# Optimization experiments

Hardware: AMD Instinct MI355X
Metric: run time of the kernel (lower is better)

Reference implementation:

```python
import jax, jax.numpy as jnp
import numpy as np

B, S, H, NH = 2, 2048, 1024, 16
HD = H // NH  # 64
SCALE = HD ** -0.5


def setup_inputs() -> dict:
    key = jax.random.key(0)
    k1, k2, k3 = jax.random.split(key, 3)
    x = jax.random.normal(k1, (B, S, H), dtype=jnp.float32)
    w_qkv = jax.random.normal(k2, (H, 3 * H), dtype=jnp.float32) * (H ** -0.5)
    b_qkv = jnp.zeros((3 * H,), dtype=jnp.float32)
    w_out = jax.random.normal(k3, (H, H), dtype=jnp.float32) * (H ** -0.5)
    b_out = jnp.zeros((H,), dtype=jnp.float32)
    return {"x": x, "w_qkv": w_qkv, "b_qkv": b_qkv, "w_out": w_out, "b_out": b_out}


def reference(x, w_qkv, b_qkv, w_out, b_out):
    # qkv projection: [B,S,3H] -> split -> [B,NH,S,HD] each
    qkv = x @ w_qkv + b_qkv
    q, k, v = jnp.split(qkv, 3, axis=-1)
    def heads(t):
        return t.reshape(B, S, NH, HD).transpose(0, 2, 1, 3)  # [B,NH,S,HD]
    q, k, v = heads(q), heads(k), heads(v)
    # full (non-causal) softmax attention; chunking in the original is
    # math-equivalent since each query row attends over all keys
    scores = jnp.einsum('bhqd,bhkd->bhqk', q, k) * SCALE
    attn = jax.nn.softmax(scores, axis=-1)
    out = jnp.einsum('bhqk,bhkd->bhqd', attn, v)  # [B,NH,S,HD]
    out = out.transpose(0, 2, 1, 3).reshape(B, S, H)
    # to_out linear (Dropout is identity in eval mode)
    return out @ w_out + b_out
```

## Files before the change

kernel.cpp:

```cpp
#include <hip/hip_runtime.h>
#include <cstdint>

using u16 = unsigned short;
typedef __bf16 bf16x8 __attribute__((ext_vector_type(8)));
typedef __bf16 bf16x4 __attribute__((ext_vector_type(4)));
typedef float f32x4 __attribute__((ext_vector_type(4)));

#define MFMA16(a, b, c) __builtin_amdgcn_mfma_f32_16x16x32_bf16((a), (b), (c), 0, 0, 0)

__device__ __forceinline__ u16 f2bf(float f) {
  union { float f; uint32_t u; } c; c.f = f;
  uint32_t u = c.u;
  u += 0x7fffu + ((u >> 16) & 1u);
  return (u16)(u >> 16);
}

#if __has_builtin(__builtin_amdgcn_global_load_lds)
#define GLOAD_LDS16(g, l)                                                      \
  __builtin_amdgcn_global_load_lds(                                            \
      (__attribute__((address_space(1))) void*)(g),                            \
      (__attribute__((address_space(3))) void*)(l), 16, 0, 0)
#else
#define GLOAD_LDS16(g, l) do { *(uint4*)(l) = *(const uint4*)(g); } while (0)
#endif

__global__ __launch_bounds__(256) void prep(
    const float* __restrict__ x, const float* __restrict__ w_qkv,
    const float* __restrict__ w_out, u16* __restrict__ xb,
    u16* __restrict__ wqT, u16* __restrict__ woT) {
  const int bid = blockIdx.x, tid = threadIdx.x;
  if (bid < 4096) {
    int i = (bid * 256 + tid) * 4;
    float4 v = *(const float4*)&x[i];
    ushort4 p;
    p.x = f2bf(v.x); p.y = f2bf(v.y); p.z = f2bf(v.z); p.w = f2bf(v.w);
    *(ushort4*)&xb[i] = p;
    return;
  }
  __shared__ float tile[32][33];
  int t = bid - 4096;
  const float* in;
  u16* outp;
  int C, bx, by;
  if (t < 3072) { in = w_qkv; outp = wqT; C = 3072; bx = (t % 96) * 32; by = (t / 96) * 32; }
  else { t -= 3072; in = w_out; outp = woT; C = 1024; bx = (t % 32) * 32; by = (t / 32) * 32; }
  const int R = 1024;
  const int tx = tid & 31, ty = tid >> 5;
#pragma unroll
  for (int r2 = 0; r2 < 4; ++r2)
    tile[ty + r2 * 8][tx] = in[(size_t)(by + ty + r2 * 8) * C + bx + tx];
  __syncthreads();
#pragma unroll
  for (int r2 = 0; r2 < 4; ++r2)
    outp[(size_t)(bx + ty + r2 * 8) * R + by + tx] = f2bf(tile[tx][ty + r2 * 8]);
}

__global__ __launch_bounds__(256, 3) void gemm_qkv(
    const u16* __restrict__ A, const u16* __restrict__ Bt,
    const float* __restrict__ bias,
    u16* __restrict__ qb, u16* __restrict__ kb, u16* __restrict__ vb,
    int M, int N, int K) {
  __shared__ u16 As[128 * 32];
  __shared__ u16 Bs[128 * 32];
  const int tid = threadIdx.x;
  const int m0 = blockIdx.x * 128;
  const int n0 = blockIdx.y * 128;
  const int lane = tid & 63, w = tid >> 6;
  const int quad = lane >> 4, l16 = lane & 15;
  const int wr = w >> 1, wc = w & 1;

  f32x4 acc[4][4] = {};

  const int r0 = tid >> 2, p0 = tid & 3;
  const int r1 = r0 + 64;
  const int c8 = p0 ^ ((r0 >> 1) & 3);
  const u16* ga0 = A + (size_t)(m0 + r0) * K + c8 * 8;
  const u16* ga1 = A + (size_t)(m0 + r1) * K + c8 * 8;
  const u16* gb0 = Bt + (size_t)(n0 + r0) * K + c8 * 8;
  const u16* gb1 = Bt + (size_t)(n0 + r1) * K + c8 * 8;
  u16* la0 = &As[tid * 8];
  u16* la1 = &As[(tid + 256) * 8];
  u16* lb0 = &Bs[tid * 8];
  u16* lb1 = &Bs[(tid + 256) * 8];

  int aoff[4], boff[4];
#pragma unroll
  for (int i = 0; i < 4; ++i) {
    int ra = wr * 64 + i * 16 + l16;
    aoff[i] = (ra * 4 + (quad ^ ((ra >> 1) & 3))) * 8;
    int rb = wc * 64 + i * 16 + l16;
    boff[i] = (rb * 4 + (quad ^ ((rb >> 1) & 3))) * 8;
  }

  const int nIter = K >> 5;
  for (int kt = 0; kt < nIter; ++kt) {
    __syncthreads();
    const int kk = kt << 5;
    GLOAD_LDS16(ga0 + kk, la0);
    GLOAD_LDS16(ga1 + kk, la1);
    GLOAD_LDS16(gb0 + kk, lb0);
    GLOAD_LDS16(gb1 + kk, lb1);
    __syncthreads();
    bf16x8 af[4], bfr[4];
#pragma unroll
    for (int i = 0; i < 4; ++i) af[i] = *(const bf16x8*)&As[aoff[i]];
#pragma unroll
    for (int j = 0; j < 4; ++j) bfr[j] = *(const bf16x8*)&Bs[boff[j]];
#pragma unroll
    for (int i = 0; i < 4; ++i)
#pragma unroll
      for (int j = 0; j < 4; ++j)
        acc[i][j] = MFMA16(af[i], bfr[j], acc[i][j]);
  }

  const int S = 2048, NH = 16;
#pragma unroll
  for (int i = 0; i < 4; ++i) {
    const int mb = m0 + wr * 64 + i * 16 + quad * 4;
#pragma unroll
    for (int j = 0; j < 4; ++j) {
      const int n = n0 + wc * 64 + j * 16 + l16;
      const float bv = bias[n];
      const int which = n >> 10;
      const int hn = n & 1023;
      const int h = hn >> 6, d = hn & 63;
      const int b = mb >> 11, s = mb & 2047;
      const int bh = b * NH + h;
      if (which == 2) {
        ushort4 pk;
        pk.x = f2bf(acc[i][j][0] + bv);
        pk.y = f2bf(acc[i][j][1] + bv);
        pk.z = f2bf(acc[i][j][2] + bv);
        pk.w = f2bf(acc[i][j][3] + bv);
        *(ushort4*)&vb[((size_t)bh * 64 + d) * S + s] = pk;
      } else {
        const float sc = (which == 0) ? 0.18033688f : 1.0f;
        u16* dst = (which == 0) ? qb : kb;
#pragma unroll
        for (int r = 0; r < 4; ++r)
          dst[((size_t)bh * S + s + r) * 64 + d] = f2bf((acc[i][j][r] + bv) * sc);
      }
    }
  }
}

__global__ __launch_bounds__(256, 2) void gemm_out(
    const u16* __restrict__ A, const u16* __restrict__ Bt,
    const float* __restrict__ bias, float* __restrict__ outf,
    int M, int N, int K) {
  __shared__ u16 As[64 * 32];
  __shared__ u16 Bs[128 * 32];
  const int tid = threadIdx.x;
  const int m0 = blockIdx.x * 64;
  const int n0 = blockIdx.y * 128;
  const int lane = tid & 63, w = tid >> 6;
  const int quad = lane >> 4, l16 = lane & 15;
  const int wr = w >> 1, wc = w & 1;

  f32x4 acc[2][4] = {};

  const int r0 = tid >> 2, p0 = tid & 3;
  const int c8 = p0 ^ ((r0 >> 1) & 3);
  const u16* ga0 = A + (size_t)(m0 + r0) * K + c8 * 8;
  const u16* gb0 = Bt + (size_t)(n0 + r0) * K + c8 * 8;
  const u16* gb1 = Bt + (size_t)(n0 + r0 + 64) * K + c8 * 8;
  u16* la0 = &As[tid * 8];
  u16* lb0 = &Bs[tid * 8];
  u16* lb1 = &Bs[(tid + 256) * 8];

  int aoff[2], boff[4];
#pragma unroll
  for (int i = 0; i < 2; ++i) {
    int ra = wr * 32 + i * 16 + l16;
    aoff[i] = (ra * 4 + (quad ^ ((ra >> 1) & 3))) * 8;
  }
#pragma unroll
  for (int j = 0; j < 4; ++j) {
    int rb = wc * 64 + j * 16 + l16;
    boff[j] = (rb * 4 + (quad ^ ((rb >> 1) & 3))) * 8;
  }

  const int nIter = K >> 5;
  for (int kt = 0; kt < nIter; ++kt) {
    __syncthreads();
    const int kk = kt << 5;
    GLOAD_LDS16(ga0 + kk, la0);
    GLOAD_LDS16(gb0 + kk, lb0);
    GLOAD_LDS16(gb1 + kk, lb1);
    __syncthreads();
    bf16x8 af[2], bfr[4];
#pragma unroll
    for (int i = 0; i < 2; ++i) af[i] = *(const bf16x8*)&As[aoff[i]];
#pragma unroll
    for (int j = 0; j < 4; ++j) bfr[j] = *(const bf16x8*)&Bs[boff[j]];
#pragma unroll
    for (int i = 0; i < 2; ++i)
#pragma unroll
      for (int j = 0; j < 4; ++j)
        acc[i][j] = MFMA16(af[i], bfr[j], acc[i][j]);
  }

#pragma unroll
  for (int i = 0; i < 2; ++i) {
    const int mb = m0 + wr * 32 + i * 16 + quad * 4;
#pragma unroll
    for (int j = 0; j < 4; ++j) {
      const int n = n0 + wc * 64 + j * 16 + l16;
      const float bv = bias[n];
#pragma unroll
      for (int r = 0; r < 4; ++r)
        outf[(size_t)(mb + r) * N + n] = acc[i][j][r] + bv;
    }
  }
}

__global__ __launch_bounds__(256, 2) void attn_fa(
    const u16* __restrict__ qg, const u16* __restrict__ kg,
    const u16* __restrict__ vg, u16* __restrict__ o) {
  const int S = 2048, NH = 16;
  const int h = blockIdx.x, b = blockIdx.y, qblk = blockIdx.z;
  const int bh = b * NH + h;
  const int tid = threadIdx.x, w = tid >> 6, lane = tid & 63;
  const int quad = lane >> 4, l16 = lane & 15;

  __shared__ u16 Ks[2][4096];
  __shared__ u16 Vs[2][4096];
  __shared__ u16 Ps[4][2048];

  const int q0 = qblk * 128 + w * 32;
  const u16* qp = qg + ((size_t)bh * S + q0 + l16) * 64 + quad * 8;
  const bf16x8 qf00 = *(const bf16x8*)qp;
  const bf16x8 qf01 = *(const bf16x8*)(qp + 32);
  const bf16x8 qf10 = *(const bf16x8*)(qp + 1024);
  const bf16x8 qf11 = *(const bf16x8*)(qp + 1024 + 32);

  f32x4 accO0[4] = {}, accO1[4] = {};
  f32x4 accL0 = {}, accL1 = {};

  bf16x8 ones;
#pragma unroll
  for (int i = 0; i < 8; ++i) ones[i] = (__bf16)1.0f;

  const u16* kbase = kg + (size_t)bh * S * 64;
  const u16* vbase = vg + (size_t)bh * 64 * S;

  const int sr0 = tid >> 3, sp0 = tid & 7;
  const int c8s = sp0 ^ (sr0 & 7);
  const u16* kS0 = kbase + (size_t)sr0 * 64 + c8s * 8;
  const u16* kS1 = kbase + (size_t)(sr0 + 32) * 64 + c8s * 8;
  const u16* vS0 = vbase + (size_t)sr0 * S + c8s * 8;
  const u16* vS1 = vbase + (size_t)(sr0 + 32) * S + c8s * 8;

  int koff[4][2];
#pragma unroll
  for (int ct = 0; ct < 4; ++ct) {
    int row = ct * 16 + l16;
    koff[ct][0] = (row * 8 + (quad ^ (row & 7))) * 8;
    koff[ct][1] = (row * 8 + ((quad + 4) ^ (row & 7))) * 8;
  }
  u16* Pw0 = &Ps[w][l16 * 64];
  u16* Pw1 = Pw0 + 1024;
  int pgx[4];
#pragma unroll
  for (int ct = 0; ct < 4; ++ct) pgx[ct] = ((ct * 4 + quad) ^ l16) * 4;
  const int pr0 = ((quad * 2) ^ l16) * 4;

  GLOAD_LDS16(kS0, &Ks[0][tid * 8]);
  GLOAD_LDS16(kS1, &Ks[0][tid * 8 + 2048]);
  GLOAD_LDS16(vS0, &Vs[0][tid * 8]);
  GLOAD_LDS16(vS1, &Vs[0][tid * 8 + 2048]);

  for (int kt = 0; kt < S / 64; ++kt) {
    const int cur = kt & 1;
    __syncthreads();
    if (kt + 1 < S / 64) {
      const int nb = cur ^ 1;
      GLOAD_LDS16(kS0 + (size_t)(kt + 1) * 4096, &Ks[nb][tid * 8]);
      GLOAD_LDS16(kS1 + (size_t)(kt + 1) * 4096, &Ks[nb][tid * 8 + 2048]);
      GLOAD_LDS16(vS0 + (kt + 1) * 64, &Vs[nb][tid * 8]);
      GLOAD_LDS16(vS1 + (kt + 1) * 64, &Vs[nb][tid * 8 + 2048]);
    }
    const u16* Kc = Ks[cur];
    const u16* Vc = Vs[cur];

    bf16x8 kf0[4], kf1[4];
#pragma unroll
    for (int ct = 0; ct < 4; ++ct) {
      kf0[ct] = *(const bf16x8*)&Kc[koff[ct][0]];
      kf1[ct] = *(const bf16x8*)&Kc[koff[ct][1]];
    }
    f32x4 s0[4] = {}, s1[4] = {};
#pragma unroll
    for (int ct = 0; ct < 4; ++ct) {
      s0[ct] = MFMA16(kf0[ct], qf00, s0[ct]);
      s0[ct] = MFMA16(kf1[ct], qf01, s0[ct]);
      s1[ct] = MFMA16(kf0[ct], qf10, s1[ct]);
      s1[ct] = MFMA16(kf1[ct], qf11, s1[ct]);
    }

#pragma unroll
    for (int ct = 0; ct < 4; ++ct)
#pragma unroll
      for (int r = 0; r < 4; ++r) {
        s0[ct][r] = __builtin_amdgcn_exp2f(s0[ct][r]);
        s1[ct][r] = __builtin_amdgcn_exp2f(s1[ct][r]);
      }

#pragma unroll
    for (int ct = 0; ct < 4; ++ct) {
      bf16x4 a = {(__bf16)s0[ct][0], (__bf16)s0[ct][1],
                  (__bf16)s0[ct][2], (__bf16)s0[ct][3]};
      *(bf16x4*)&Pw0[pgx[ct]] = a;
      bf16x4 c = {(__bf16)s1[ct][0], (__bf16)s1[ct][1],
                  (__bf16)s1[ct][2], (__bf16)s1[ct][3]};
      *(bf16x4*)&Pw1[pgx[ct]] = c;
    }

    bf16x4 t0 = *(const bf16x4*)&Pw0[pr0];
    bf16x4 t1 = *(const bf16x4*)&Pw0[pr0 ^ 4];
    bf16x4 t2 = *(const bf16x4*)&Pw0[pr0 ^ 32];
    bf16x4 t3 = *(const bf16x4*)&Pw0[pr0 ^ 36];
    bf16x8 pf00 = __builtin_shufflevector(t0, t1, 0, 1, 2, 3, 4, 5, 6, 7);
    bf16x8 pf01 = __builtin_shufflevector(t2, t3, 0, 1, 2, 3, 4, 5, 6, 7);
    t0 = *(const bf16x4*)&Pw1[pr0];
    t1 = *(const bf16x4*)&Pw1[pr0 ^ 4];
    t2 = *(const bf16x4*)&Pw1[pr0 ^ 32];
    t3 = *(const bf16x4*)&Pw1[pr0 ^ 36];
    bf16x8 pf10 = __builtin_shufflevector(t0, t1, 0, 1, 2, 3, 4, 5, 6, 7);
    bf16x8 pf11 = __builtin_shufflevector(t2, t3, 0, 1, 2, 3, 4, 5, 6, 7);

    accL0 = MFMA16(ones, pf00, accL0);
    accL0 = MFMA16(ones, pf01, accL0);
    accL1 = MFMA16(ones, pf10, accL1);
    accL1 = MFMA16(ones, pf11, accL1);

#pragma unroll
    for (int ct = 0; ct < 4; ++ct) {
      bf16x8 vf0 = *(const bf16x8*)&Vc[koff[ct][0]];
      bf16x8 vf1 = *(const bf16x8*)&Vc[koff[ct][1]];
      accO0[ct] = MFMA16(vf0, pf00, accO0[ct]);
      accO0[ct] = MFMA16(vf1, pf01, accO0[ct]);
      accO1[ct] = MFMA16(vf0, pf10, accO1[ct]);
      accO1[ct] = MFMA16(vf1, pf11, accO1[ct]);
    }
  }

  const float inv0 = 1.f / accL0[0], inv1 = 1.f / accL1[0];

  const int s0r = q0 + l16, s1r = q0 + 16 + l16;
#pragma unroll
  for (int ct = 0; ct < 4; ++ct) {
    ushort4 pk;
    pk.x = f2bf(accO0[ct][0] * inv0);
    pk.y = f2bf(accO0[ct][1] * inv0);
    pk.z = f2bf(accO0[ct][2] * inv0);
    pk.w = f2bf(accO0[ct][3] * inv0);
    *(ushort4*)&o[(size_t)(b * S + s0r) * 1024 + h * 64 + ct * 16 + quad * 4] = pk;
    pk.x = f2bf(accO1[ct][0] * inv1);
    pk.y = f2bf(accO1[ct][1] * inv1);
    pk.z = f2bf(accO1[ct][2] * inv1);
    pk.w = f2bf(accO1[ct][3] * inv1);
    *(ushort4*)&o[(size_t)(b * S + s1r) * 1024 + h * 64 + ct * 16 + quad * 4] = pk;
  }
}


extern "C" void kernel_launch(void* const* d_in, const int* in_sizes, int n_in,
                              void* d_out, int out_size, void* d_ws, size_t ws_size,
                              hipStream_t stream) {
  const float* x = (const float*)d_in[0];
  const float* w_qkv = (const float*)d_in[1];
  const float* b_qkv = (const float*)d_in[2];
  const float* w_out = (const float*)d_in[3];
  const float* b_out = (const float*)d_in[4];
  float* out = (float*)d_out;

  u16* xb = (u16*)d_ws;
  u16* wqT = xb + 4096 * 1024;
  u16* woT = wqT + 3072 * 1024;
  u16* qb = woT + 1024 * 1024;
  u16* kb = qb + 4194304;
  u16* vb = kb + 4194304;
  u16* ao = vb + 4194304;

  prep<<<8192, 256, 0, stream>>>(x, w_qkv, w_out, xb, wqT, woT);
  gemm_qkv<<<dim3(32, 24), 256, 0, stream>>>(xb, wqT, b_qkv, qb, kb, vb,
                                             4096, 3072, 1024);
  attn_fa<<<dim3(16, 2, 16), 256, 0, stream>>>(qb, kb, vb, ao);
  gemm_out<<<dim3(64, 8), 256, 0, stream>>>(ao, woT, b_out, out,
                                            4096, 1024, 1024);
}
```

Measured before the change: 183.8 us.

## Fuse all stages into one persistent cooperative kernel with grid syncs

Replaces the four separate launches (prep, QKV GEMM, flash attention, output GEMM) with a single persistent cooperative kernel. Blocks loop over work items and stages are separated by grid.sync. The QKV GEMM tile also changes to 128x192, giving 512 tiles. The aim is to remove launch gaps and per-kernel tail effects, at the cost of grid-wide barrier overhead, occupancy limited by 2 blocks per CU, and shared memory sized for the largest stage. If the cooperative launch fails, it falls back to the original four launches.

```diff
diff --git a/kernel.cpp b/kernel.cpp
--- a/kernel.cpp
+++ b/kernel.cpp
@@ -1,5 +1,8 @@
 #include <hip/hip_runtime.h>
+#include <hip/hip_cooperative_groups.h>
 #include <cstdint>
+
+namespace cg = cooperative_groups;
 
 using u16 = unsigned short;
 typedef __bf16 bf16x8 __attribute__((ext_vector_type(8)));
@@ -23,6 +26,351 @@
 #else
 #define GLOAD_LDS16(g, l) do { *(uint4*)(l) = *(const uint4*)(g); } while (0)
 #endif
+
+__global__ __launch_bounds__(256, 2) void fused(
+    const float* __restrict__ x, const float* __restrict__ w_qkv,
+    const float* __restrict__ b_qkv, const float* __restrict__ w_out,
+    const float* __restrict__ b_out, float* __restrict__ out,
+    u16* __restrict__ xb, u16* __restrict__ wqT, u16* __restrict__ woT,
+    u16* __restrict__ qb, u16* __restrict__ kb, u16* __restrict__ vb,
+    u16* __restrict__ ao) {
+  const int S = 2048;
+  const int tid = threadIdx.x;
+  const int lane = tid & 63, w = tid >> 6;
+  const int quad = lane >> 4, l16 = lane & 15;
+
+  __shared__ __align__(16) u16 smem[24576];
+  cg::grid_group grid = cg::this_grid();
+
+  for (int v = blockIdx.x; v < 8192; v += gridDim.x) {
+    if (v < 4096) {
+      int i = (v * 256 + tid) * 4;
+      float4 vv = *(const float4*)&x[i];
+      ushort4 p;
+      p.x = f2bf(vv.x); p.y = f2bf(vv.y); p.z = f2bf(vv.z); p.w = f2bf(vv.w);
+      *(ushort4*)&xb[i] = p;
+    } else {
+      float* tile = (float*)smem;
+      int t = v - 4096;
+      const float* in;
+      u16* outp;
+      int C, bx, by;
+      if (t < 3072) { in = w_qkv; outp = wqT; C = 3072; bx = (t % 96) * 32; by = (t / 96) * 32; }
+      else { t -= 3072; in = w_out; outp = woT; C = 1024; bx = (t % 32) * 32; by = (t / 32) * 32; }
+      const int tx = tid & 31, ty = tid >> 5;
+      __syncthreads();
+#pragma unroll
+      for (int r2 = 0; r2 < 4; ++r2)
+        tile[(ty + r2 * 8) * 33 + tx] = in[(size_t)(by + ty + r2 * 8) * C + bx + tx];
+      __syncthreads();
+#pragma unroll
+      for (int r2 = 0; r2 < 4; ++r2)
+        outp[(size_t)(bx + ty + r2 * 8) * 1024 + by + tx] = f2bf(tile[tx * 33 + ty + r2 * 8]);
+    }
+  }
+  __threadfence();
+  grid.sync();
+  __threadfence();
+
+  for (int p = blockIdx.x; p < 512; p += gridDim.x) {
+    u16* As = smem;
+    u16* Bs = smem + 4096;
+    const int m0 = (p & 31) * 128;
+    const int n0 = (p >> 5) * 192;
+    const int wr = w >> 1, wc = w & 1;
+
+    f32x4 acc[4][6] = {};
+
+    const int r0 = tid >> 2, p0 = tid & 3;
+    const int c8 = p0 ^ ((r0 >> 1) & 3);
+    const u16* ga0 = xb + (size_t)(m0 + r0) * 1024 + c8 * 8;
+    const u16* ga1 = ga0 + (size_t)64 * 1024;
+    const u16* gb0 = wqT + (size_t)(n0 + r0) * 1024 + c8 * 8;
+    const u16* gb1 = gb0 + (size_t)64 * 1024;
+    const u16* gb2 = gb0 + (size_t)128 * 1024;
+    u16* la0 = &As[tid * 8];
+    u16* la1 = &As[(tid + 256) * 8];
+    u16* lb0 = &Bs[tid * 8];
+    u16* lb1 = &Bs[(tid + 256) * 8];
+    u16* lb2 = &Bs[(tid + 512) * 8];
+
+    int aoff[4], boff[6];
+#pragma unroll
+    for (int i = 0; i < 4; ++i) {
+      int ra = wr * 64 + i * 16 + l16;
+      aoff[i] = (ra * 4 + (quad ^ ((ra >> 1) & 3))) * 8;
+    }
+#pragma unroll
+    for (int j = 0; j < 6; ++j) {
+      int rb = wc * 96 + j * 16 + l16;
+      boff[j] = (rb * 4 + (quad ^ ((rb >> 1) & 3))) * 8;
+    }
+
+    for (int kt = 0; kt < 32; ++kt) {
+      __syncthreads();
+      const int kk = kt << 5;
+      GLOAD_LDS16(ga0 + kk, la0);
+      GLOAD_LDS16(ga1 + kk, la1);
+      GLOAD_LDS16(gb0 + kk, lb0);
+      GLOAD_LDS16(gb1 + kk, lb1);
+      GLOAD_LDS16(gb2 + kk, lb2);
+      __syncthreads();
+      bf16x8 af[4], bfr[6];
+#pragma unroll
+      for (int i = 0; i < 4; ++i) af[i] = *(const bf16x8*)&As[aoff[i]];
+#pragma unroll
+      for (int j = 0; j < 6; ++j) bfr[j] = *(const bf16x8*)&Bs[boff[j]];
+#pragma unroll
+      for (int i = 0; i < 4; ++i)
+#pragma unroll
+        for (int j = 0; j < 6; ++j)
+          acc[i][j] = MFMA16(af[i], bfr[j], acc[i][j]);
+    }
+
+#pragma unroll
+    for (int i = 0; i < 4; ++i) {
+      const int mb = m0 + wr * 64 + i * 16 + quad * 4;
+#pragma unroll
+      for (int j = 0; j < 6; ++j) {
+        const int n = n0 + wc * 96 + j * 16 + l16;
+        const float bv = b_qkv[n];
+        const int which = n >> 10;
+        const int hn = n & 1023;
+        const int hh = hn >> 6, d = hn & 63;
+        const int bb = mb >> 11, s = mb & 2047;
+        const int bh = bb * 16 + hh;
+        if (which == 2) {
+          ushort4 pk;
+          pk.x = f2bf(acc[i][j][0] + bv);
+          pk.y = f2bf(acc[i][j][1] + bv);
+          pk.z = f2bf(acc[i][j][2] + bv);
+          pk.w = f2bf(acc[i][j][3] + bv);
+          *(ushort4*)&vb[((size_t)bh * 64 + d) * S + s] = pk;
+        } else {
+          const float sc = (which == 0) ? 0.18033688f : 1.0f;
+          u16* dst = (which == 0) ? qb : kb;
+#pragma unroll
+          for (int r = 0; r < 4; ++r)
+            dst[((size_t)bh * S + s + r) * 64 + d] = f2bf((acc[i][j][r] + bv) * sc);
+        }
+      }
+    }
+  }
+  __threadfence();
+  grid.sync();
+  __threadfence();
+
+  for (int p = blockIdx.x; p < 512; p += gridDim.x) {
+    u16* KsB = smem;
+    u16* VsB = smem + 8192;
+    u16* PsB = smem + 16384;
+    const int ah = p & 15, ab = (p >> 4) & 1, qblk = p >> 5;
+    const int bh = ab * 16 + ah;
+
+    const int q0 = qblk * 128 + w * 32;
+    const u16* qp = qb + ((size_t)bh * S + q0 + l16) * 64 + quad * 8;
+    const bf16x8 qf00 = *(const bf16x8*)qp;
+    const bf16x8 qf01 = *(const bf16x8*)(qp + 32);
+    const bf16x8 qf10 = *(const bf16x8*)(qp + 1024);
+    const bf16x8 qf11 = *(const bf16x8*)(qp + 1024 + 32);
+
+    f32x4 accO0[4] = {}, accO1[4] = {};
+    f32x4 accL0 = {}, accL1 = {};
+
+    bf16x8 ones;
+#pragma unroll
+    for (int i = 0; i < 8; ++i) ones[i] = (__bf16)1.0f;
+
+    const u16* kbase = kb + (size_t)bh * S * 64;
+    const u16* vbase = vb + (size_t)bh * 64 * S;
+
+    const int sr0 = tid >> 3, sp0 = tid & 7;
+    const int c8s = sp0 ^ (sr0 & 7);
+    const u16* kS0 = kbase + (size_t)sr0 * 64 + c8s * 8;
+    const u16* kS1 = kbase + (size_t)(sr0 + 32) * 64 + c8s * 8;
+    const u16* vS0 = vbase + (size_t)sr0 * S + c8s * 8;
+    const u16* vS1 = vbase + (size_t)(sr0 + 32) * S + c8s * 8;
+
+    int koff[4][2];
+#pragma unroll
+    for (int ct = 0; ct < 4; ++ct) {
+      int row = ct * 16 + l16;
+      koff[ct][0] = (row * 8 + (quad ^ (row & 7))) * 8;
+      koff[ct][1] = (row * 8 + ((quad + 4) ^ (row & 7))) * 8;
+    }
+    u16* Pw0 = &PsB[w * 2048 + l16 * 64];
+    u16* Pw1 = Pw0 + 1024;
+    int pgx[4];
+#pragma unroll
+    for (int ct = 0; ct < 4; ++ct) pgx[ct] = ((ct * 4 + quad) ^ l16) * 4;
+    const int pr0 = ((quad * 2) ^ l16) * 4;
+
+    __syncthreads();
+    GLOAD_LDS16(kS0, &KsB[tid * 8]);
+    GLOAD_LDS16(kS1, &KsB[tid * 8 + 2048]);
+    GLOAD_LDS16(vS0, &VsB[tid * 8]);
+    GLOAD_LDS16(vS1, &VsB[tid * 8 + 2048]);
+
+    for (int kt = 0; kt < S / 64; ++kt) {
+      const int cur = kt & 1;
+      __syncthreads();
+      if (kt + 1 < S / 64) {
+        const int nb = cur ^ 1;
+        GLOAD_LDS16(kS0 + (size_t)(kt + 1) * 4096, &KsB[nb * 4096 + tid * 8]);
+        GLOAD_LDS16(kS1 + (size_t)(kt + 1) * 4096, &KsB[nb * 4096 + tid * 8 + 2048]);
+        GLOAD_LDS16(vS0 + (kt + 1) * 64, &VsB[nb * 4096 + tid * 8]);
+        GLOAD_LDS16(vS1 + (kt + 1) * 64, &VsB[nb * 4096 + tid * 8 + 2048]);
+      }
+      const u16* Kc = KsB + cur * 4096;
+      const u16* Vc = VsB + cur * 4096;
+
+      bf16x8 kf0[4], kf1[4];
+#pragma unroll
+      for (int ct = 0; ct < 4; ++ct) {
+        kf0[ct] = *(const bf16x8*)&Kc[koff[ct][0]];
+        kf1[ct] = *(const bf16x8*)&Kc[koff[ct][1]];
+      }
+      f32x4 s0[4] = {}, s1[4] = {};
+#pragma unroll
+      for (int ct = 0; ct < 4; ++ct) {
+        s0[ct] = MFMA16(kf0[ct], qf00, s0[ct]);
+        s0[ct] = MFMA16(kf1[ct], qf01, s0[ct]);
+        s1[ct] = MFMA16(kf0[ct], qf10, s1[ct]);
+        s1[ct] = MFMA16(kf1[ct], qf11, s1[ct]);
+      }
+
+#pragma unroll
+      for (int ct = 0; ct < 4; ++ct)
+#pragma unroll
+        for (int r = 0; r < 4; ++r) {
+          s0[ct][r] = __builtin_amdgcn_exp2f(s0[ct][r]);
+          s1[ct][r] = __builtin_amdgcn_exp2f(s1[ct][r]);
+        }
+
+#pragma unroll
+      for (int ct = 0; ct < 4; ++ct) {
+        bf16x4 a = {(__bf16)s0[ct][0], (__bf16)s0[ct][1],
+                    (__bf16)s0[ct][2], (__bf16)s0[ct][3]};
+        *(bf16x4*)&Pw0[pgx[ct]] = a;
+        bf16x4 c = {(__bf16)s1[ct][0], (__bf16)s1[ct][1],
+                    (__bf16)s1[ct][2], (__bf16)s1[ct][3]};
+        *(bf16x4*)&Pw1[pgx[ct]] = c;
+      }
+
+      bf16x4 t0 = *(const bf16x4*)&Pw0[pr0];
+      bf16x4 t1 = *(const bf16x4*)&Pw0[pr0 ^ 4];
+      bf16x4 t2 = *(const bf16x4*)&Pw0[pr0 ^ 32];
+      bf16x4 t3 = *(const bf16x4*)&Pw0[pr0 ^ 36];
+      bf16x8 pf00 = __builtin_shufflevector(t0, t1, 0, 1, 2, 3, 4, 5, 6, 7);
+      bf16x8 pf01 = __builtin_shufflevector(t2, t3, 0, 1, 2, 3, 4, 5, 6, 7);
+      t0 = *(const bf16x4*)&Pw1[pr0];
+      t1 = *(const bf16x4*)&Pw1[pr0 ^ 4];
+      t2 = *(const bf16x4*)&Pw1[pr0 ^ 32];
+      t3 = *(const bf16x4*)&Pw1[pr0 ^ 36];
+      bf16x8 pf10 = __builtin_shufflevector(t0, t1, 0, 1, 2, 3, 4, 5, 6, 7);
+      bf16x8 pf11 = __builtin_shufflevector(t2, t3, 0, 1, 2, 3, 4, 5, 6, 7);
+
+      accL0 = MFMA16(ones, pf00, accL0);
+      accL0 = MFMA16(ones, pf01, accL0);
+      accL1 = MFMA16(ones, pf10, accL1);
+      accL1 = MFMA16(ones, pf11, accL1);
+
+#pragma unroll
+      for (int ct = 0; ct < 4; ++ct) {
+        bf16x8 vf0 = *(const bf16x8*)&Vc[koff[ct][0]];
+        bf16x8 vf1 = *(const bf16x8*)&Vc[koff[ct][1]];
+        accO0[ct] = MFMA16(vf0, pf00, accO0[ct]);
+        accO0[ct] = MFMA16(vf1, pf01, accO0[ct]);
+        accO1[ct] = MFMA16(vf0, pf10, accO1[ct]);
+        accO1[ct] = MFMA16(vf1, pf11, accO1[ct]);
+      }
+    }
+
+    const float inv0 = 1.f / accL0[0], inv1 = 1.f / accL1[0];
+    const int s0r = q0 + l16, s1r = q0 + 16 + l16;
+#pragma unroll
+    for (int ct = 0; ct < 4; ++ct) {
+      ushort4 pk;
+      pk.x = f2bf(accO0[ct][0] * inv0);
+      pk.y = f2bf(accO0[ct][1] * inv0);
+      pk.z = f2bf(accO0[ct][2] * inv0);
+      pk.w = f2bf(accO0[ct][3] * inv0);
+      *(ushort4*)&ao[(size_t)(ab * S + s0r) * 1024 + ah * 64 + ct * 16 + quad * 4] = pk;
+      pk.x = f2bf(accO1[ct][0] * inv1);
+      pk.y = f2bf(accO1[ct][1] * inv1);
+      pk.z = f2bf(accO1[ct][2] * inv1);
+      pk.w = f2bf(accO1[ct][3] * inv1);
+      *(ushort4*)&ao[(size_t)(ab * S + s1r) * 1024 + ah * 64 + ct * 16 + quad * 4] = pk;
+    }
+  }
+  __threadfence();
+  grid.sync();
+  __threadfence();
+
+  for (int p = blockIdx.x; p < 512; p += gridDim.x) {
+    u16* As = smem;
+    u16* Bs = smem + 2048;
+    const int m0 = (p & 63) * 64;
+    const int n0 = (p >> 6) * 128;
+    const int wr = w >> 1, wc = w & 1;
+
+    f32x4 acc[2][4] = {};
+
+    const int r0 = tid >> 2, p0 = tid & 3;
+    const int c8 = p0 ^ ((r0 >> 1) & 3);
+    const u16* ga0 = ao + (size_t)(m0 + r0) * 1024 + c8 * 8;
+    const u16* gb0 = woT + (size_t)(n0 + r0) * 1024 + c8 * 8;
+    const u16* gb1 = gb0 + (size_t)64 * 1024;
+    u16* la0 = &As[tid * 8];
+    u16* lb0 = &Bs[tid * 8];
+    u16* lb1 = &Bs[(tid + 256) * 8];
+
+    int aoff[2], boff[4];
+#pragma unroll
+    for (int i = 0; i < 2; ++i) {
+      int ra = wr * 32 + i * 16 + l16;
+      aoff[i] = (ra * 4 + (quad ^ ((ra >> 1) & 3))) * 8;
+    }
+#pragma unroll
+    for (int j = 0; j < 4; ++j) {
+      int rb = wc * 64 + j * 16 + l16;
+      boff[j] = (rb * 4 + (quad ^ ((rb >> 1) & 3))) * 8;
+    }
+
+    for (int kt = 0; kt < 32; ++kt) {
+      __syncthreads();
+      const int kk = kt << 5;
+      GLOAD_LDS16(ga0 + kk, la0);
+      GLOAD_LDS16(gb0 + kk, lb0);
+      GLOAD_LDS16(gb1 + kk, lb1);
+      __syncthreads();
+      bf16x8 af[2], bfr[4];
+#pragma unroll
+      for (int i = 0; i < 2; ++i) af[i] = *(const bf16x8*)&As[aoff[i]];
+#pragma unroll
+      for (int j = 0; j < 4; ++j) bfr[j] = *(const bf16x8*)&Bs[boff[j]];
+#pragma unroll
+      for (int i = 0; i < 2; ++i)
+#pragma unroll
+        for (int j = 0; j < 4; ++j)
+          acc[i][j] = MFMA16(af[i], bfr[j], acc[i][j]);
+    }
+
+#pragma unroll
+    for (int i = 0; i < 2; ++i) {
+      const int mb = m0 + wr * 32 + i * 16 + quad * 4;
+#pragma unroll
+      for (int j = 0; j < 4; ++j) {
+        const int n = n0 + wc * 64 + j * 16 + l16;
+        const float bv = b_out[n];
+#pragma unroll
+        for (int r = 0; r < 4; ++r)
+          out[(size_t)(mb + r) * 1024 + n] = acc[i][j][r] + bv;
+      }
+    }
+  }
+}
+
 
 __global__ __launch_bounds__(256) void prep(
     const float* __restrict__ x, const float* __restrict__ w_qkv,
@@ -44,7 +392,6 @@
   int C, bx, by;
   if (t < 3072) { in = w_qkv; outp = wqT; C = 3072; bx = (t % 96) * 32; by = (t / 96) * 32; }
   else { t -= 3072; in = w_out; outp = woT; C = 1024; bx = (t % 32) * 32; by = (t / 32) * 32; }
-  const int R = 1024;
   const int tx = tid & 31, ty = tid >> 5;
 #pragma unroll
   for (int r2 = 0; r2 < 4; ++r2)
@@ -52,7 +399,7 @@
   __syncthreads();
 #pragma unroll
   for (int r2 = 0; r2 < 4; ++r2)
-    outp[(size_t)(bx + ty + r2 * 8) * R + by + tx] = f2bf(tile[tx][ty + r2 * 8]);
+    outp[(size_t)(bx + ty + r2 * 8) * 1024 + by + tx] = f2bf(tile[tx][ty + r2 * 8]);
 }
 
 __global__ __launch_bounds__(256, 3) void gemm_qkv(
@@ -383,10 +730,24 @@
   u16* vb = kb + 4194304;
   u16* ao = vb + 4194304;
 
-  prep<<<8192, 256, 0, stream>>>(x, w_qkv, w_out, xb, wqT, woT);
-  gemm_qkv<<<dim3(32, 24), 256, 0, stream>>>(xb, wqT, b_qkv, qb, kb, vb,
-                                             4096, 3072, 1024);
-  attn_fa<<<dim3(16, 2, 16), 256, 0, stream>>>(qb, kb, vb, ao);
-  gemm_out<<<dim3(64, 8), 256, 0, stream>>>(ao, woT, b_out, out,
-                                            4096, 1024, 1024);
+  int perCU = 0;
+  hipError_t err = hipOccupancyMaxActiveBlocksPerMultiprocessor(&perCU, fused,
+                                                                256, 0);
+  int nblk = (err == hipSuccess && perCU > 0) ? perCU * 256 : 512;
+  if (nblk > 512) nblk = 512;
+
+  void* args[] = {(void*)&x, (void*)&w_qkv, (void*)&b_qkv, (void*)&w_out,
+                  (void*)&b_out, (void*)&out, (void*)&xb, (void*)&wqT,
+                  (void*)&woT, (void*)&qb, (void*)&kb, (void*)&vb, (void*)&ao};
+  err = hipLaunchCooperativeKernel(fused, dim3(nblk), dim3(256), args, 0,
+                                   stream);
+  if (err != hipSuccess) {
+    (void)hipGetLastError();
+    prep<<<8192, 256, 0, stream>>>(x, w_qkv, w_out, xb, wqT, woT);
+    gemm_qkv<<<dim3(32, 24), 256, 0, stream>>>(xb, wqT, b_qkv, qb, kb, vb,
+                                               4096, 3072, 1024);
+    attn_fa<<<dim3(16, 2, 16), 256, 0, stream>>>(qb, kb, vb, ao);
+    gemm_out<<<dim3(64, 8), 256, 0, stream>>>(ao, woT, b_out, out,
+                                              4096, 1024, 1024);
+  }
 }
```

After: 458.8 us. +149.6%, slower.
